# Optimization experiments

Hardware: AMD Instinct MI355X
Metric: run time of the kernel (lower is better)

## Reference

```python
import jax, jax.numpy as jnp
import numpy as np
from jax import lax

BOX_STRIDES = (32, 64, 128, 256)
MASK_STRIDE = 4
MASK_SIZE = 28
PATCH = 512
TOPK = 64
SCORE_TH = 0.5
IOU_TH = 0.5
MASK_TH = 0.5


def setup_inputs():
    key = jax.random.key(0)
    ks = jax.random.split(key, 10)
    d = {}
    d["pred0"] = jax.random.normal(ks[0], (2, 6, 16, 16), jnp.float32)
    d["pred1"] = jax.random.normal(ks[1], (2, 6, 8, 8), jnp.float32)
    d["pred2"] = jax.random.normal(ks[2], (2, 6, 4, 4), jnp.float32)
    d["pred3"] = jax.random.normal(ks[3], (2, 6, 2, 2), jnp.float32)
    d["feat0"] = jax.random.normal(ks[4], (2, 64, 128, 128), jnp.float32)
    d["feat1"] = jax.random.normal(ks[5], (2, 64, 64, 64), jnp.float32)
    d["feat2"] = jax.random.normal(ks[6], (2, 64, 32, 32), jnp.float32)
    d["feat3"] = jax.random.normal(ks[7], (2, 64, 16, 16), jnp.float32)
    d["w1"] = jax.random.normal(ks[8], (128, 256, 3, 3), jnp.float32) * 0.05
    d["b1"] = jnp.zeros((128,), jnp.float32)
    d["w2"] = jax.random.normal(ks[9], (1, 128, 1, 1), jnp.float32) * 0.05
    d["b2"] = jnp.zeros((1,), jnp.float32)
    return d


def _decode_level(pred, stride):
    # pred: [B, 6, H, W] -> [B, H*W, 6], (cx,cy)=(p+grid)*stride, wh=exp(p)*stride
    B, no, H, W = pred.shape
    p = pred.transpose(0, 2, 3, 1).reshape(B, H * W, no)
    gy, gx = jnp.meshgrid(jnp.arange(H), jnp.arange(W), indexing="ij")
    grid = jnp.stack([gx.ravel(), gy.ravel()], axis=-1).astype(p.dtype)  # [HW,2] (x,y)
    xy = (p[..., 0:2] + grid) * stride
    wh = jnp.exp(p[..., 2:4]) * stride
    return jnp.concatenate([xy, wh, p[..., 4:]], axis=-1)


def _iou_matrix(b):
    # b: [K,4] xyxy
    area = jnp.clip(b[:, 2] - b[:, 0], 0) * jnp.clip(b[:, 3] - b[:, 1], 0)
    ix0 = jnp.maximum(b[:, None, 0], b[None, :, 0])
    iy0 = jnp.maximum(b[:, None, 1], b[None, :, 1])
    ix1 = jnp.minimum(b[:, None, 2], b[None, :, 2])
    iy1 = jnp.minimum(b[:, None, 3], b[None, :, 3])
    inter = jnp.clip(ix1 - ix0, 0) * jnp.clip(iy1 - iy0, 0)
    union = area[:, None] + area[None, :] - inter
    return inter / jnp.maximum(union, 1e-9)


def _nms_keep(boxes, labels, valid):
    # boxes already sorted by descending score; batched NMS via per-class coord offset
    off = labels.astype(boxes.dtype)[:, None] * (PATCH * 8.0)
    iou = _iou_matrix(boxes + off)
    idx = jnp.arange(TOPK)

    def body(i, keep):
        sup = keep[i] & (iou[i] > IOU_TH) & (idx > i)
        return keep & ~sup

    return lax.fori_loop(0, TOPK, body, valid)


def _roi_align_one(feat, box):
    # feat: [C,Hf,Wf]; box: [4] xyxy in image coords (spatial_scale=1/MASK_STRIDE)
    # torchvision-style aligned=False, one bilinear sample per bin center
    C, Hf, Wf = feat.shape
    b = box / MASK_STRIDE
    bw = (b[2] - b[0]) / MASK_SIZE
    bh = (b[3] - b[1]) / MASK_SIZE
    xs = b[0] + (jnp.arange(MASK_SIZE, dtype=feat.dtype) + 0.5) * bw
    ys = b[1] + (jnp.arange(MASK_SIZE, dtype=feat.dtype) + 0.5) * bh
    x = jnp.clip(jnp.broadcast_to(xs[None, :], (MASK_SIZE, MASK_SIZE)), 0.0, Wf - 1.0)
    y = jnp.clip(jnp.broadcast_to(ys[:, None], (MASK_SIZE, MASK_SIZE)), 0.0, Hf - 1.0)
    x0 = jnp.floor(x).astype(jnp.int32)
    y0 = jnp.floor(y).astype(jnp.int32)
    x1 = jnp.minimum(x0 + 1, Wf - 1)
    y1 = jnp.minimum(y0 + 1, Hf - 1)
    fx = x - x0
    fy = y - y0
    v00 = feat[:, y0, x0]
    v01 = feat[:, y0, x1]
    v10 = feat[:, y1, x0]
    v11 = feat[:, y1, x1]
    return (v00 * (1 - fy) * (1 - fx) + v01 * (1 - fy) * fx
            + v10 * fy * (1 - fx) + v11 * fy * fx)  # [C,S,S]


def _paste_one(mask_soft, box_int):
    # nearest-neighbor upsample of [S,S] mask into its box on a [P,P] canvas
    x0, y0, x1, y1 = box_int[0], box_int[1], box_int[2], box_int[3]
    h = y1 - y0 + 1
    w = x1 - x0 + 1
    ys = jnp.arange(PATCH, dtype=jnp.int32)
    xs = jnp.arange(PATCH, dtype=jnp.int32)
    iy = jnp.clip((ys - y0) * MASK_SIZE // h, 0, MASK_SIZE - 1)
    ix = jnp.clip((xs - x0) * MASK_SIZE // w, 0, MASK_SIZE - 1)
    g = mask_soft[iy][:, ix]  # [P,P]
    inside = ((ys >= y0) & (ys <= y1))[:, None] & ((xs >= x0) & (xs <= x1))[None, :]
    return jnp.where(inside, g, 0.0)


def _conv(x, w, b, pad):
    y = lax.conv_general_dilated(x, w, (1, 1), pad, dimension_numbers=("NCHW", "OIHW", "NCHW"))
    return y + b[None, :, None, None]


def _pipeline(pred0, pred1, pred2, pred3, feat0, feat1, feat2, feat3, w1, b1, w2, b2):
    # box branch: decode per-level predictions
    yolo = jnp.concatenate(
        [_decode_level(p, s) for p, s in zip([pred0, pred1, pred2, pred3], BOX_STRIDES)],
        axis=1,
    )  # [B,N,6]
    B = yolo.shape[0]
    cx, cy, w_, h_ = yolo[..., 0], yolo[..., 1], yolo[..., 2], yolo[..., 3]
    boxes = jnp.stack([cx - w_ / 2, cy - h_ / 2, cx + w_ / 2, cy + h_ / 2], axis=-1)
    scores = jax.nn.sigmoid(yolo[..., 4])
    labels = jnp.argmax(yolo[..., 5:], axis=-1)
    valid = scores > SCORE_TH
    top_scores, top_idx = lax.top_k(jnp.where(valid, scores, 0.0), TOPK)
    boxes_k = jnp.take_along_axis(boxes, top_idx[..., None], axis=1)  # [B,K,4]
    labels_k = jnp.take_along_axis(labels, top_idx, axis=1)
    valid_k = top_scores > SCORE_TH
    keep = jax.vmap(_nms_keep)(boxes_k, labels_k, valid_k)  # [B,K] bool

    # mask branch: merge mask feats at the first level's resolution (nearest)
    H0, W0 = feat0.shape[2], feat0.shape[3]
    merged = jnp.concatenate(
        [feat0] + [jax.image.resize(f, (B, f.shape[1], H0, W0), "nearest") for f in [feat1, feat2, feat3]],
        axis=1,
    )  # [B,256,H0,W0]
    rois = jax.vmap(lambda f, bx: jax.vmap(lambda bb: _roi_align_one(f, bb))(bx))(merged, boxes_k)
    C = rois.shape[2]
    x = rois.reshape(B * TOPK, C, MASK_SIZE, MASK_SIZE)
    hdn = jax.nn.silu(_conv(x, w1, b1, "SAME"))
    logits = _conv(hdn, w2, b2, "SAME")  # [B*K,1,S,S]
    soft = jax.nn.sigmoid(logits).reshape(B, TOPK, MASK_SIZE, MASK_SIZE)

    box_int = jnp.clip(boxes_k, 0, PATCH - 1).astype(jnp.int32)
    pasted = jax.vmap(jax.vmap(_paste_one))(soft, box_int)  # [B,K,P,P]
    return top_scores, boxes_k, labels_k, pasted, keep


def reference(pred0, pred1, pred2, pred3, feat0, feat1, feat2, feat3, w1, b1, w2, b2):
    top_scores, boxes_k, labels_k, pasted, keep = _pipeline(
        pred0, pred1, pred2, pred3, feat0, feat1, feat2, feat3, w1, b1, w2, b2
    )
    out_scores = top_scores * keep
    bin_masks = (pasted > MASK_TH) & keep[:, :, None, None]
    return out_scores, boxes_k, labels_k.astype(jnp.int32), bin_masks, keep
```

## Files before the change

kernel.cpp:

```cpp
#include <hip/hip_runtime.h>
#include <hip/hip_bf16.h>
#include <cstdint>

#define NTOPK 64
#define A_TOT 340
#define MS 28

#define OFF_SCORES 0
#define OFF_BOXES  128
#define OFF_LABELS 640
#define OFF_MASKS  768
#define OFF_KEEP   33555200ull

typedef __attribute__((ext_vector_type(4))) float f32x4;
typedef long fp8x8;

__device__ __forceinline__ float sigmoidf_(float x) { return 1.f / (1.f + expf(-x)); }
__device__ __forceinline__ float bf2f(unsigned u) {
  return __uint_as_float(u << 16);
}
__device__ __forceinline__ unsigned short f2bf(float f) {
  __hip_bfloat16 h = __float2bfloat16(f);
  return *(unsigned short*)&h;
}

__global__ __launch_bounds__(256) void k_prep(
    const float* __restrict__ p0, const float* __restrict__ p1,
    const float* __restrict__ p2, const float* __restrict__ p3,
    const float* __restrict__ f0, const float* __restrict__ f1,
    const float* __restrict__ f2, const float* __restrict__ f3,
    const float* __restrict__ w1,
    float* __restrict__ out,
    float* __restrict__ ws_boxes, int* __restrict__ ws_keep,
    int* __restrict__ ws_boxint,
    unsigned char* __restrict__ wt, unsigned short* __restrict__ mg)
{
  __shared__ __align__(16) char smem_raw[128 * 260 * 2];
  const int bid = blockIdx.x;
  const int t = threadIdx.x;

  if (bid < 2) {
    const int b = bid;
    float* sc = (float*)smem_raw;
    float(*bx)[4] = (float(*)[4])(sc + A_TOT);
    float* tk_score = (float*)(bx + A_TOT);
    float(*tk_box)[4] = (float(*)[4])(tk_score + 64);

    for (int a = t; a < A_TOT; a += 256) {
      const float* pp; int W, HW, la; float stride;
      if (a < 256)      { pp = p0; W = 16; HW = 256; la = a;       stride = 32.f;  }
      else if (a < 320) { pp = p1; W = 8;  HW = 64;  la = a - 256; stride = 64.f;  }
      else if (a < 336) { pp = p2; W = 4;  HW = 16;  la = a - 320; stride = 128.f; }
      else              { pp = p3; W = 2;  HW = 4;   la = a - 336; stride = 256.f; }
      const float* base = pp + (size_t)b * 6 * HW + la;
      float v0 = base[0], v1 = base[HW], v2 = base[2 * HW], v3 = base[3 * HW], v4 = base[4 * HW];
      int gx = la % W, gy = la / W;
      float cx = (v0 + (float)gx) * stride;
      float cy = (v1 + (float)gy) * stride;
      float w_ = expf(v2) * stride;
      float h_ = expf(v3) * stride;
      float score = sigmoidf_(v4);
      sc[a] = (score > 0.5f) ? score : 0.f;
      bx[a][0] = cx - 0.5f * w_;
      bx[a][1] = cy - 0.5f * h_;
      bx[a][2] = cx + 0.5f * w_;
      bx[a][3] = cy + 0.5f * h_;
    }
    __syncthreads();

    for (int a = t; a < A_TOT; a += 256) {
      float my = sc[a];
      int rank = 0;
      for (int j = 0; j < A_TOT; ++j) {
        float o = sc[j];
        rank += (o > my) || (o == my && j < a);
      }
      if (rank < NTOPK) {
        tk_score[rank] = my;
        tk_box[rank][0] = bx[a][0];
        tk_box[rank][1] = bx[a][1];
        tk_box[rank][2] = bx[a][2];
        tk_box[rank][3] = bx[a][3];
      }
    }
    __syncthreads();

    if (t < NTOPK) {
      float x0 = tk_box[t][0], y0 = tk_box[t][1];
      float x1 = tk_box[t][2], y1 = tk_box[t][3];
      float s = tk_score[t];
      float area = fmaxf(x1 - x0, 0.f) * fmaxf(y1 - y0, 0.f);
      int keep = (s > 0.5f) ? 1 : 0;
      for (int i = 0; i < NTOPK - 1; ++i) {
        int   ki = __shfl(keep, i);
        float a0 = __shfl(x0, i);
        float c0 = __shfl(y0, i);
        float a1 = __shfl(x1, i);
        float c1 = __shfl(y1, i);
        float ai = __shfl(area, i);
        if (ki && t > i && keep) {
          float ix0 = fmaxf(a0, x0), iy0 = fmaxf(c0, y0);
          float ix1 = fminf(a1, x1), iy1 = fminf(c1, y1);
          float inter = fmaxf(ix1 - ix0, 0.f) * fmaxf(iy1 - iy0, 0.f);
          float uni = ai + area - inter;
          float iou = inter / fmaxf(uni, 1e-9f);
          if (iou > 0.5f) keep = 0;
        }
      }
      int box = b * NTOPK + t;
      out[OFF_SCORES + box] = keep ? s : 0.f;
      float bv[4] = {x0, y0, x1, y1};
      #pragma unroll
      for (int c = 0; c < 4; ++c) {
        out[OFF_BOXES + box * 4 + c] = bv[c];
        ws_boxes[box * 4 + c] = bv[c];
        float bc = fminf(fmaxf(bv[c], 0.f), 511.f);
        ws_boxint[box * 4 + c] = (int)bc;
      }
      out[OFF_LABELS + box] = 0.f;
      out[OFF_KEEP + box] = keep ? 1.f : 0.f;
      ws_keep[box] = keep;
    }
    return;
  }

  if (bid < 130) {
    const int co = bid - 2;
    const int ci = t;
    const int c = ci >> 5, cil = ci & 31;
    const int cq = co >> 5, col = co & 31;
    const int slot = ((cil >> 3) ^ ((col >> 2) & 3)) * 8 + (cil & 7);
    const float* src = w1 + ((size_t)co * 256 + ci) * 9;
    #pragma unroll
    for (int tap = 0; tap < 9; ++tap) {
      unsigned u = __builtin_amdgcn_cvt_pk_fp8_f32(src[tap], 0.f, 0, false);
      wt[(((size_t)(cq * 8 + c) * 9 + tap)) * 1024 + col * 32 + slot] =
          (unsigned char)(u & 0xff);
    }
    return;
  }

  {
    const int idx = bid - 130;
    const int b = idx >> 7;
    const int y = idx & 127;
    unsigned short* tile = (unsigned short*)smem_raw;
    const int x = t & 127, ch = t >> 7;

    {
      const float* src = f0 + ((size_t)b * 64) * 16384 + y * 128 + x;
      for (int cc = 0; cc < 32; ++cc) {
        int cl = ch * 32 + cc;
        tile[x * 260 + cl] = f2bf(src[(size_t)cl * 16384]);
      }
    }
    {
      const float* src = f1 + ((size_t)b * 64) * 4096 + (y >> 1) * 64 + (x >> 1);
      for (int cc = 0; cc < 32; ++cc) {
        int cl = ch * 32 + cc;
        tile[x * 260 + 64 + cl] = f2bf(src[(size_t)cl * 4096]);
      }
    }
    {
      const float* src = f2 + ((size_t)b * 64) * 1024 + (y >> 2) * 32 + (x >> 2);
      for (int cc = 0; cc < 32; ++cc) {
        int cl = ch * 32 + cc;
        tile[x * 260 + 128 + cl] = f2bf(src[(size_t)cl * 1024]);
      }
    }
    {
      const float* src = f3 + ((size_t)b * 64) * 256 + (y >> 3) * 16 + (x >> 3);
      for (int cc = 0; cc < 32; ++cc) {
        int cl = ch * 32 + cc;
        tile[x * 260 + 192 + cl] = f2bf(src[(size_t)cl * 256]);
      }
    }
    __syncthreads();
    unsigned short* dst = mg + (((size_t)b * 128 + y) * 128) * 256;
    for (int it = 0; it < 32; ++it) {
      int qq = t + it * 256;
      int xx = qq >> 6, cg = qq & 63;
      *(ushort4*)(dst + xx * 256 + cg * 4) = *(ushort4*)&tile[xx * 260 + cg * 4];
    }
  }
}

__global__ __launch_bounds__(256) void k_roistage(
    const unsigned short* __restrict__ mg,
    const float* __restrict__ ws_boxes, const int* __restrict__ ws_keep,
    unsigned char* __restrict__ roi)
{
  const int boxLo = blockIdx.x & 7;
  const int r2 = blockIdx.x >> 3;
  const int r = r2 % 30;
  const int box = ((r2 / 30) << 3) | boxLo;
  if (!ws_keep[box]) return;
  const int t = threadIdx.x;
  unsigned char* rbox = roi + (size_t)box * 8 * 30 * 1024;
  const int gr = r - 1;

  if (gr < 0 || gr > 27) {
    uint2 z = {0u, 0u};
    for (int e = t; e < 1024; e += 256) {
      int chunk = e >> 7, rem = e & 127;
      int cell = rem >> 2, quad = rem & 3;
      size_t off = ((size_t)(chunk * 30 + r)) * 1024 + cell * 32 +
                   (quad ^ ((cell >> 2) & 3)) * 8;
      *(uint2*)(rbox + off) = z;
    }
    return;
  }

  __shared__ int   xa_s[MS], xb_s[MS];
  __shared__ float fx_s[MS];
  __shared__ float by_s[4];
  if (t < 4) by_s[t] = ws_boxes[box * 4 + t];
  __syncthreads();
  const float b0 = by_s[0] * 0.25f, b1_ = by_s[1] * 0.25f;
  const float b2_ = by_s[2] * 0.25f, b3_ = by_s[3] * 0.25f;
  if (t < MS) {
    float bw = (b2_ - b0) * (1.f / MS);
    float x = b0 + ((float)t + 0.5f) * bw;
    x = fminf(fmaxf(x, 0.f), 127.f);
    int x0 = (int)floorf(x);
    xa_s[t] = x0; xb_s[t] = min(x0 + 1, 127); fx_s[t] = x - (float)x0;
  }
  float bh = (b3_ - b1_) * (1.f / MS);
  float yy = b1_ + ((float)gr + 0.5f) * bh;
  yy = fminf(fmaxf(yy, 0.f), 127.f);
  int ya = (int)floorf(yy);
  int yb = min(ya + 1, 127);
  float fy = yy - (float)ya;
  __syncthreads();

  const int b = box >> 6;
  const unsigned short* mgb = mg + ((size_t)b * 128 * 128) * 256;

  for (int e = t; e < 1024; e += 256) {
    int chunk = e >> 7, rem = e & 127;
    int cell = rem >> 2, quad = rem & 3;
    size_t off = ((size_t)(chunk * 30 + r)) * 1024 + cell * 32 +
                 (quad ^ ((cell >> 2) & 3)) * 8;
    int gc = cell - 1;
    if (gc < 0 || gc > 27) {
      uint2 z = {0u, 0u};
      *(uint2*)(rbox + off) = z;
      continue;
    }
    int U = chunk * 4 + quad;
    int xa = xa_s[gc], xb = xb_s[gc];
    float fx = fx_s[gc];
    float w00 = (1.f - fy) * (1.f - fx), w01 = (1.f - fy) * fx;
    float w10 = fy * (1.f - fx),         w11 = fy * fx;
    uint4 A = *(const uint4*)(mgb + ((size_t)(ya * 128 + xa)) * 256 + U * 8);
    uint4 B = *(const uint4*)(mgb + ((size_t)(ya * 128 + xb)) * 256 + U * 8);
    uint4 C = *(const uint4*)(mgb + ((size_t)(yb * 128 + xa)) * 256 + U * 8);
    uint4 D = *(const uint4*)(mgb + ((size_t)(yb * 128 + xb)) * 256 + U * 8);
    const unsigned* pa = (const unsigned*)&A;
    const unsigned* pb = (const unsigned*)&B;
    const unsigned* pc = (const unsigned*)&C;
    const unsigned* pd = (const unsigned*)&D;
    float f[8];
    #pragma unroll
    for (int k2 = 0; k2 < 4; ++k2) {
      f[2 * k2] = bf2f(pa[k2] & 0xffffu) * w00 + bf2f(pb[k2] & 0xffffu) * w01 +
                  bf2f(pc[k2] & 0xffffu) * w10 + bf2f(pd[k2] & 0xffffu) * w11;
      f[2 * k2 + 1] = bf2f(pa[k2] >> 16) * w00 + bf2f(pb[k2] >> 16) * w01 +
                      bf2f(pc[k2] >> 16) * w10 + bf2f(pd[k2] >> 16) * w11;
    }
    unsigned o0 = __builtin_amdgcn_cvt_pk_fp8_f32(f[0], f[1], 0, false);
    o0 = __builtin_amdgcn_cvt_pk_fp8_f32(f[2], f[3], o0, true);
    unsigned o1 = __builtin_amdgcn_cvt_pk_fp8_f32(f[4], f[5], 0, false);
    o1 = __builtin_amdgcn_cvt_pk_fp8_f32(f[6], f[7], o1, true);
    uint2 pk; pk.x = o0; pk.y = o1;
    *(uint2*)(rbox + off) = pk;
  }
}

__global__ __launch_bounds__(256, 4) void k_conv(
    const unsigned char* __restrict__ roi,
    const unsigned char* __restrict__ wt,
    const float* __restrict__ b1, const float* __restrict__ w2,
    const int* __restrict__ ws_keep,
    float* __restrict__ ws_logit4)
{
  const int bid = blockIdx.x;
  const int boxLo = bid & 7;
  const int r1 = bid >> 3;
  const int cq = r1 & 3;
  const int q = (r1 >> 2) & 3;
  const int box = ((r1 >> 4) << 3) | boxLo;
  if (!ws_keep[box]) return;
  const int t = threadIdx.x;
  const int lane = t & 63, wv = t >> 6;
  const int laneN = lane & 15, kg = lane >> 4;

  const int rot = (wv + (bid >> 3)) & 3;

  __shared__ __align__(16) unsigned char lds[2][9216];

  int badd[4][3];
  bool act[4];
  #pragma unroll
  for (int i = 0; i < 4; ++i) {
    int tile = rot + 4 * i;
    act[i] = (tile * 16) < 196;
    int p = tile * 16 + laneN;
    if (p > 195) p = 195;
    int py = p / 28, px = p - py * 28;
    #pragma unroll
    for (int dx = 0; dx < 3; ++dx) {
      int cell = px + dx;
      badd[i][dx] = py * 1024 + cell * 32 + (kg ^ ((cell >> 2) & 3)) * 8;
    }
  }
  const int aswz = (kg ^ ((laneN >> 2) & 3)) * 8;

  f32x4 acc[2][4];
  #pragma unroll
  for (int m = 0; m < 2; ++m)
    #pragma unroll
    for (int i = 0; i < 4; ++i) acc[m][i] = (f32x4){0.f, 0.f, 0.f, 0.f};

  const uint4* rbase = (const uint4*)roi;
  const unsigned char* wbase = wt + (size_t)cq * 8 * 9216;

  uint4 gb0, gb1, gb2;
  auto issue_load = [&](int c) {
    const uint4* s = rbase + ((size_t)(box * 8 + c) * 30 + q * 7) * 64;
    gb0 = s[t]; gb1 = s[t + 256];
    if (t < 64) gb2 = s[t + 512];
  };
  auto write_lds = [&](int buf) {
    uint4* db = (uint4*)lds[buf];
    db[t] = gb0; db[t + 256] = gb1;
    if (t < 64) db[t + 512] = gb2;
  };

  issue_load(0);
  write_lds(0);
  __syncthreads();

  int cur = 0;
  #pragma unroll 1
  for (int c = 0; c < 8; ++c) {
    if (c < 7) issue_load(c + 1);
    const unsigned char* wa = wbase + (size_t)c * 9216;
    const unsigned char* bb = lds[cur];
    #pragma unroll
    for (int tap = 0; tap < 9; ++tap) {
      const int dy = tap / 3, dx = tap % 3;
      fp8x8 av0 = *(const fp8x8*)(wa + tap * 1024 + laneN * 32 + aswz);
      fp8x8 av1 = *(const fp8x8*)(wa + tap * 1024 + 512 + laneN * 32 + aswz);
      #pragma unroll
      for (int i = 0; i < 4; ++i) {
        if (act[i]) {
          fp8x8 bv = *(const fp8x8*)(bb + badd[i][dx] + dy * 1024);
          acc[0][i] = __builtin_amdgcn_mfma_f32_16x16x32_fp8_fp8(av0, bv, acc[0][i], 0, 0, 0);
          acc[1][i] = __builtin_amdgcn_mfma_f32_16x16x32_fp8_fp8(av1, bv, acc[1][i], 0, 0, 0);
        }
      }
    }
    if (c < 7) {
      write_lds(cur ^ 1);
      __syncthreads();
      cur ^= 1;
    }
  }

  float b1v[2][4], w2v[2][4];
  #pragma unroll
  for (int m = 0; m < 2; ++m)
    #pragma unroll
    for (int r = 0; r < 4; ++r) {
      int co = cq * 32 + m * 16 + kg * 4 + r;
      b1v[m][r] = b1[co];
      w2v[m][r] = w2[co];
    }
  #pragma unroll
  for (int i = 0; i < 4; ++i) {
    if (!act[i]) continue;
    float part = 0.f;
    #pragma unroll
    for (int m = 0; m < 2; ++m)
      #pragma unroll
      for (int r = 0; r < 4; ++r) {
        float h = acc[m][i][r] + b1v[m][r];
        part = fmaf(w2v[m][r], h * sigmoidf_(h), part);
      }
    part += __shfl_xor(part, 16);
    part += __shfl_xor(part, 32);
    int p = (rot + 4 * i) * 16 + laneN;
    if (kg == 0 && p < 196)
      ws_logit4[((size_t)box * 4 + cq) * 784 + q * 196 + p] = part;
  }
}

__global__ __launch_bounds__(256) void k_paste(
    const float* __restrict__ ws_logit4, const int* __restrict__ ws_keep,
    const int* __restrict__ ws_boxint, const float* __restrict__ b2,
    float* __restrict__ out)
{
  const int box = blockIdx.x >> 4;
  const int yo  = blockIdx.x & 15;
  const int t = threadIdx.x;
  float* mb = out + OFF_MASKS + (size_t)box * 262144 + (size_t)yo * 32 * 512;

  if (!ws_keep[box]) {
    f32x4 z = {0.f, 0.f, 0.f, 0.f};
    f32x4* p = (f32x4*)mb;
    for (int e = t; e < 4096; e += 256)
      __builtin_nontemporal_store(z, p + e);
    return;
  }

  __shared__ float soft[784];
  __shared__ int iys[32];
  __shared__ int bi[4];
  if (t < 4) bi[t] = ws_boxint[box * 4 + t];
  __syncthreads();
  const int x0 = bi[0], y0 = bi[1], x1 = bi[2], y1 = bi[3];
  const int w = x1 - x0 + 1, h = y1 - y0 + 1;
  const float b2v = b2[0];
  const float* l0 = ws_logit4 + (size_t)box * 4 * 784;

  for (int e = t; e < 784; e += 256)
    soft[e] = sigmoidf_(l0[e] + l0[784 + e] + l0[1568 + e] + l0[2352 + e] + b2v);
  if (t < 32) {
    int Y = yo * 32 + t;
    int vy = (Y - y0) * MS;
    int iy = (vy >= 0) ? (vy / h) : 0;
    iys[t] = min(max(iy, 0), MS - 1);
  }
  __syncthreads();

  const int c4 = (t & 127) * 4;
  const int rr = t >> 7;
  int ixr[4];
  bool inx[4];
  #pragma unroll
  for (int u = 0; u < 4; ++u) {
    int X = c4 + u;
    int vx = (X - x0) * MS;
    int ix = (vx >= 0) ? (vx / w) : 0;
    ixr[u] = min(max(ix, 0), MS - 1);
    inx[u] = (X >= x0) && (X <= x1);
  }

  int prev_iy = -1;
  f32x4 v = {0.f, 0.f, 0.f, 0.f};
  #pragma unroll 1
  for (int it = 0; it < 16; ++it) {
    int Yl = it * 2 + rr;
    int Y = yo * 32 + Yl;
    f32x4 o;
    if (Y >= y0 && Y <= y1) {
      int iy = iys[Yl];
      if (iy != prev_iy) {
        prev_iy = iy;
        #pragma unroll
        for (int u = 0; u < 4; ++u)
          v[u] = (inx[u] && soft[iy * MS + ixr[u]] > 0.5f) ? 1.f : 0.f;
      }
      o = v;
    } else {
      o = (f32x4){0.f, 0.f, 0.f, 0.f};
    }
    __builtin_nontemporal_store(o, (f32x4*)(mb + (size_t)Yl * 512 + c4));
  }
}

extern "C" void kernel_launch(void* const* d_in, const int* in_sizes, int n_in,
                              void* d_out, int out_size, void* d_ws, size_t ws_size,
                              hipStream_t stream) {
  const float* p0 = (const float*)d_in[0];
  const float* p1 = (const float*)d_in[1];
  const float* p2 = (const float*)d_in[2];
  const float* p3 = (const float*)d_in[3];
  const float* f0 = (const float*)d_in[4];
  const float* f1 = (const float*)d_in[5];
  const float* f2 = (const float*)d_in[6];
  const float* f3 = (const float*)d_in[7];
  const float* w1 = (const float*)d_in[8];
  const float* b1 = (const float*)d_in[9];
  const float* w2 = (const float*)d_in[10];
  const float* b2 = (const float*)d_in[11];
  float* out = (float*)d_out;

  float* wsf = (float*)d_ws;
  float*          ws_boxes  = wsf;
  int*            ws_keep   = (int*)(wsf + 512);
  int*            ws_boxint = (int*)(wsf + 640);
  float*          ws_logit4 = wsf + 1152;
  unsigned char*  ws_wt     = (unsigned char*)(wsf + 402560);
  unsigned short* ws_merged = (unsigned short*)(wsf + 476288);
  unsigned char*  ws_roi    = (unsigned char*)(wsf + 4670592);

  k_prep<<<386, 256, 0, stream>>>(p0, p1, p2, p3, f0, f1, f2, f3, w1,
                                  out, ws_boxes, ws_keep, ws_boxint,
                                  ws_wt, ws_merged);
  k_roistage<<<3840, 256, 0, stream>>>(ws_merged, ws_boxes, ws_keep, ws_roi);
  k_conv<<<2048, 256, 0, stream>>>(ws_roi, ws_wt, b1, w2, ws_keep, ws_logit4);
  k_paste<<<2048, 256, 0, stream>>>(ws_logit4, ws_keep, ws_boxint, b2, out);
}
```

Before: 271.4 us.

## Give each conv wave one output-channel quarter over all pixel tiles

```diff
diff --git a/kernel.cpp b/kernel.cpp
--- a/kernel.cpp
+++ b/kernel.cpp
@@ -277,7 +277,7 @@
   }
 }
 
-__global__ __launch_bounds__(256, 4) void k_conv(
+__global__ __launch_bounds__(256, 2) void k_conv(
     const unsigned char* __restrict__ roi,
     const unsigned char* __restrict__ wt,
     const float* __restrict__ b1, const float* __restrict__ w2,
@@ -287,40 +287,31 @@
   const int bid = blockIdx.x;
   const int boxLo = bid & 7;
   const int r1 = bid >> 3;
-  const int cq = r1 & 3;
-  const int q = (r1 >> 2) & 3;
-  const int box = ((r1 >> 4) << 3) | boxLo;
+  const int q = r1 & 3;
+  const int box = ((r1 >> 2) << 3) | boxLo;
   if (!ws_keep[box]) return;
   const int t = threadIdx.x;
-  const int lane = t & 63, wv = t >> 6;
+  const int lane = t & 63, cq = t >> 6;
   const int laneN = lane & 15, kg = lane >> 4;
 
-  const int rot = (wv + (bid >> 3)) & 3;
-
   __shared__ __align__(16) unsigned char lds[2][9216];
 
-  int badd[4][3];
-  bool act[4];
+  int rowb[13], pxv[13];
   #pragma unroll
-  for (int i = 0; i < 4; ++i) {
-    int tile = rot + 4 * i;
-    act[i] = (tile * 16) < 196;
-    int p = tile * 16 + laneN;
+  for (int i = 0; i < 13; ++i) {
+    int p = i * 16 + laneN;
     if (p > 195) p = 195;
-    int py = p / 28, px = p - py * 28;
-    #pragma unroll
-    for (int dx = 0; dx < 3; ++dx) {
-      int cell = px + dx;
-      badd[i][dx] = py * 1024 + cell * 32 + (kg ^ ((cell >> 2) & 3)) * 8;
-    }
+    int py = p / 28;
+    pxv[i] = p - py * 28;
+    rowb[i] = py * 1024;
   }
   const int aswz = (kg ^ ((laneN >> 2) & 3)) * 8;
 
-  f32x4 acc[2][4];
+  f32x4 acc[2][13];
   #pragma unroll
   for (int m = 0; m < 2; ++m)
     #pragma unroll
-    for (int i = 0; i < 4; ++i) acc[m][i] = (f32x4){0.f, 0.f, 0.f, 0.f};
+    for (int i = 0; i < 13; ++i) acc[m][i] = (f32x4){0.f, 0.f, 0.f, 0.f};
 
   const uint4* rbase = (const uint4*)roi;
   const unsigned char* wbase = wt + (size_t)cq * 8 * 9216;
@@ -344,21 +335,25 @@
   int cur = 0;
   #pragma unroll 1
   for (int c = 0; c < 8; ++c) {
+    const unsigned char* wa = wbase + (size_t)c * 9216;
+    fp8x8 av0[9], av1[9];
+    #pragma unroll
+    for (int tap = 0; tap < 9; ++tap) {
+      av0[tap] = *(const fp8x8*)(wa + tap * 1024 + laneN * 32 + aswz);
+      av1[tap] = *(const fp8x8*)(wa + tap * 1024 + 512 + laneN * 32 + aswz);
+    }
     if (c < 7) issue_load(c + 1);
-    const unsigned char* wa = wbase + (size_t)c * 9216;
     const unsigned char* bb = lds[cur];
     #pragma unroll
     for (int tap = 0; tap < 9; ++tap) {
-      const int dy = tap / 3, dx = tap % 3;
-      fp8x8 av0 = *(const fp8x8*)(wa + tap * 1024 + laneN * 32 + aswz);
-      fp8x8 av1 = *(const fp8x8*)(wa + tap * 1024 + 512 + laneN * 32 + aswz);
+      const int dy = tap / 3, dx = tap - dy * 3;
       #pragma unroll
-      for (int i = 0; i < 4; ++i) {
-        if (act[i]) {
-          fp8x8 bv = *(const fp8x8*)(bb + badd[i][dx] + dy * 1024);
-          acc[0][i] = __builtin_amdgcn_mfma_f32_16x16x32_fp8_fp8(av0, bv, acc[0][i], 0, 0, 0);
-          acc[1][i] = __builtin_amdgcn_mfma_f32_16x16x32_fp8_fp8(av1, bv, acc[1][i], 0, 0, 0);
-        }
+      for (int i = 0; i < 13; ++i) {
+        int cell = pxv[i] + dx;
+        fp8x8 bv = *(const fp8x8*)(bb + rowb[i] + dy * 1024 + cell * 32 +
+                                   ((kg ^ ((cell >> 2) & 3)) << 3));
+        acc[0][i] = __builtin_amdgcn_mfma_f32_16x16x32_fp8_fp8(av0[tap], bv, acc[0][i], 0, 0, 0);
+        acc[1][i] = __builtin_amdgcn_mfma_f32_16x16x32_fp8_fp8(av1[tap], bv, acc[1][i], 0, 0, 0);
       }
     }
     if (c < 7) {
@@ -378,8 +373,7 @@
       w2v[m][r] = w2[co];
     }
   #pragma unroll
-  for (int i = 0; i < 4; ++i) {
-    if (!act[i]) continue;
+  for (int i = 0; i < 13; ++i) {
     float part = 0.f;
     #pragma unroll
     for (int m = 0; m < 2; ++m)
@@ -390,7 +384,7 @@
       }
     part += __shfl_xor(part, 16);
     part += __shfl_xor(part, 32);
-    int p = (rot + 4 * i) * 16 + laneN;
+    int p = i * 16 + laneN;
     if (kg == 0 && p < 196)
       ws_logit4[((size_t)box * 4 + cq) * 784 + q * 196 + p] = part;
   }
@@ -500,6 +494,6 @@
                                   out, ws_boxes, ws_keep, ws_boxint,
                                   ws_wt, ws_merged);
   k_roistage<<<3840, 256, 0, stream>>>(ws_merged, ws_boxes, ws_keep, ws_roi);
-  k_conv<<<2048, 256, 0, stream>>>(ws_roi, ws_wt, b1, w2, ws_keep, ws_logit4);
+  k_conv<<<512, 256, 0, stream>>>(ws_roi, ws_wt, b1, w2, ws_keep, ws_logit4);
   k_paste<<<2048, 256, 0, stream>>>(ws_logit4, ws_keep, ws_boxint, b2, out);
 }
```

Measured after the change: 333.4 us. 1.23x slower.
